# Performance work log

Measured on AMD Instinct MI355X. Metric: run time of the kernel, lower is better.

Reference implementation:

```python
import jax, jax.numpy as jnp
import numpy as np

N, E = 20000, 320000
C, IN_NF, HID_NF, OUT_NF, CH_NF, RAD_NF = 14, 128, 128, 128, 16, 128
CONSTANT = 1.0
LN_EPS = 1e-5
SCALE = 0.02


def _pool_matrix(c, dtype):
    # RollerPooling buffer: pool_matrix[i] averages a sliding window of size c-i
    ones = np.ones((c, c), dtype=np.float32)
    mats = [(np.triu(ones) - np.triu(ones, k=c - i)) / float(c - i) for i in range(c)]
    return jnp.asarray(np.stack(mats), dtype=dtype)


def setup_inputs() -> dict:
    key = jax.random.key(0)
    ks = jax.random.split(key, 32)
    h = jax.random.normal(ks[0], (N, IN_NF), jnp.float32)
    x = jax.random.normal(ks[1], (N, C, 3), jnp.float32)
    row = jax.random.randint(ks[2], (E,), 0, N)
    off = jax.random.randint(ks[3], (E,), 1, N)
    col = (row + off) % N  # guarantees row != col (avoids zero-distance edges)
    channel_attr = jax.random.normal(ks[4], (N, C, CH_NF), jnp.float32)
    w = jax.random.uniform(ks[5], (N, C), jnp.float32, 0.1, 1.0)
    keep = jax.random.uniform(ks[6], (N, C)) > 0.3
    keep = keep.at[:, 0].set(True)  # every node has >=1 active channel
    channel_weights = w * keep.astype(jnp.float32)

    def lin(k, o, i):
        k1, k2 = jax.random.split(k)
        return (jax.random.normal(k1, (o, i), jnp.float32) * SCALE,
                jax.random.normal(k2, (o,), jnp.float32) * SCALE)

    radial_W, radial_b = lin(ks[7], RAD_NF, CH_NF * CH_NF)
    e1_W, e1_b = lin(ks[8], HID_NF, 2 * IN_NF + RAD_NF)
    e2_W, e2_b = lin(ks[9], HID_NF, HID_NF)
    att_W, att_b = lin(ks[10], 1, HID_NF)
    c1_W, c1_b = lin(ks[11], HID_NF, HID_NF)
    c2_W, c2_b = lin(ks[12], C, HID_NF)
    n1_W, n1_b = lin(ks[13], HID_NF, IN_NF + HID_NF)
    n2_W, n2_b = lin(ks[14], OUT_NF, HID_NF)
    ln_g = jnp.ones((OUT_NF,), jnp.float32)
    ln_b = jnp.zeros((OUT_NF,), jnp.float32)
    return dict(h=h, x=x, row=row, col=col, channel_attr=channel_attr,
                channel_weights=channel_weights,
                radial_W=radial_W, radial_b=radial_b,
                e1_W=e1_W, e1_b=e1_b, e2_W=e2_W, e2_b=e2_b,
                att_W=att_W, att_b=att_b,
                c1_W=c1_W, c1_b=c1_b, c2_W=c2_W, c2_b=c2_b,
                n1_W=n1_W, n1_b=n1_b, n2_W=n2_W, n2_b=n2_b,
                ln_g=ln_g, ln_b=ln_b)


def _scatter_mean(v, idx, n):
    s = jnp.zeros((n,) + v.shape[1:], v.dtype).at[idx].add(v)
    cnt = jnp.zeros((n,), v.dtype).at[idx].add(1.0)
    cnt = jnp.maximum(cnt, 1.0)
    return s / cnt.reshape((n,) + (1,) * (v.ndim - 1))


def _forward(h, x, row, col, channel_attr, channel_weights,
             radial_W, radial_b, e1_W, e1_b, e2_W, e2_b, att_W, att_b,
             c1_W, c1_b, c2_W, c2_b, n1_W, n1_b, n2_W, n2_b, ln_g, ln_b):
    n, c, d = x.shape
    silu = jax.nn.silu
    coord_r = x[row]           # [E, C, 3]
    coord_c = x[col]
    # pairwise channel distances [E, C, C]
    dist = jnp.linalg.norm(coord_r[:, :, None, :] - coord_c[:, None, :, :], axis=-1)
    cw_r = channel_weights[row]
    cw_c = channel_weights[col]
    coord_msg = dist * (cw_r[:, :, None] * cw_c[:, None, :])
    # attr_r^T @ coord_msg @ attr_c -> [E, CH_NF, CH_NF]
    radial = jnp.einsum('eca,ecd,edb->eab', channel_attr[row], coord_msg, channel_attr[col])
    radial = radial.reshape(radial.shape[0], -1)
    rnorm = jnp.linalg.norm(radial, axis=-1, keepdims=True) + CONSTANT
    radial = (radial @ radial_W.T + radial_b) / rnorm  # [E, RAD_NF]
    # pooled column coord over active channels
    mask = (channel_weights != 0).astype(x.dtype)      # [N, C]
    csum = mask.sum(-1)                                # [N]
    pooled_col = (coord_c * mask[col][:, :, None]).sum(1) / csum[col][:, None]  # [E, 3]
    coord_diff = coord_r - pooled_col[:, None, :]      # [E, C, 3]
    # edge MLP (dropout = identity in eval)
    ef = jnp.concatenate([h[row], h[col], radial], axis=-1)
    ef = silu(ef @ e1_W.T + e1_b)
    ef = silu(ef @ e2_W.T + e2_b)
    ef = ef * jax.nn.sigmoid(ef @ att_W.T + att_b)     # att_mlp (hidden_nf == input_nf)
    # coord MLP + roller pooling
    ch = silu(ef @ c1_W.T + c1_b) @ c2_W.T + c2_b      # [E, C]
    tsize = csum[row].astype(jnp.int32) - 1            # [E] in [0, C-1]
    pool_mat = _pool_matrix(c, x.dtype)                # [C, C, C]
    pooled = jnp.einsum('eij,ej->ei', pool_mat[tsize], ch)  # [E, C]
    trans = coord_diff * pooled[:, :, None]            # [E, C, 3]
    x_out = x + _scatter_mean(trans, row, n)
    agg = _scatter_mean(ef, col, n)
    nh = jnp.concatenate([h, agg], axis=-1)
    nh = silu(nh @ n1_W.T + n1_b) @ n2_W.T + n2_b
    y = h + nh
    mu = y.mean(-1, keepdims=True)
    var = ((y - mu) ** 2).mean(-1, keepdims=True)
    h_out = (y - mu) / jnp.sqrt(var + LN_EPS) * ln_g + ln_b
    return h_out, x_out


def reference(h, x, row, col, channel_attr, channel_weights,
              radial_W, radial_b, e1_W, e1_b, e2_W, e2_b, att_W, att_b,
              c1_W, c1_b, c2_W, c2_b, n1_W, n1_b, n2_W, n2_b, ln_g, ln_b):
    return _forward(h, x, row, col, channel_attr, channel_weights,
                    radial_W, radial_b, e1_W, e1_b, e2_W, e2_b, att_W, att_b,
                    c1_W, c1_b, c2_W, c2_b, n1_W, n1_b, n2_W, n2_b, ln_g, ln_b)
```

## Files before the change

kernel.cpp:

```cpp
#include <hip/hip_runtime.h>
#include <math.h>

#define NN 20000
#define NE 320000

typedef const float* fp;
typedef short short8 __attribute__((ext_vector_type(8)));
typedef short short4v __attribute__((ext_vector_type(4)));
typedef float f32x4 __attribute__((ext_vector_type(4)));

__device__ __forceinline__ short F2B(float f) {
    unsigned u = __float_as_uint(f);
    return (short)((u + 0x7fffu + ((u >> 16) & 1u)) >> 16);
}
__device__ __forceinline__ short F2Bf(float f) {
    return (short)((__float_as_uint(f) + 0x8000u) >> 16);
}
__device__ __forceinline__ float B2F(short s) {
    return __uint_as_float(((unsigned)(unsigned short)s) << 16);
}
__device__ __forceinline__ float siluf(float v) { return v / (1.f + __expf(-v)); }

#if defined(__has_builtin)
#if __has_builtin(__builtin_amdgcn_mfma_f32_16x16x16bf16_1k)
#define MFMA16_BUILTIN 1
__device__ __forceinline__ f32x4 mfma16(short4v a, short4v b, f32x4 c) {
    return __builtin_amdgcn_mfma_f32_16x16x16bf16_1k(a, b, c, 0, 0, 0);
}
#elif __has_builtin(__builtin_amdgcn_mfma_f32_16x16x16_bf16)
#define MFMA16_BUILTIN 1
__device__ __forceinline__ f32x4 mfma16(short4v a, short4v b, f32x4 c) {
    return __builtin_amdgcn_mfma_f32_16x16x16_bf16(a, b, c, 0, 0, 0);
}
#endif
#endif
#ifndef MFMA16_BUILTIN
__device__ __forceinline__ f32x4 mfma16(short4v a, short4v b, f32x4 c) {
    f32x4 d;
    asm volatile("s_nop 1\n\tv_mfma_f32_16x16x16_bf16 %0, %1, %2, %3\n\ts_nop 7\n\ts_nop 7"
                 : "=v"(d) : "v"(a), "v"(b), "v"(c));
    return d;
}
#endif

__global__ void k_prep_w(fp e1W, fp e2W, fp c1W, fp c2W, fp n1W, fp n2W,
                         short* __restrict__ wb) {
    int i = blockIdx.x * 256 + threadIdx.x;
    if (i >= 149504) return;
    if (i >= 32768 && i < 65536) return;
    float v;
    if (i < 32768)       { int o = i >> 8, k = i & 255; v = e1W[o * 384 + k]; }
    else if (i < 81920)  v = e2W[i - 65536];
    else if (i < 98304)  v = c1W[i - 81920];
    else if (i < 100352) { int q = i - 98304; v = (q < 1792) ? c2W[q] : 0.f; }
    else if (i < 133120) v = n1W[i - 100352];
    else                 v = n2W[i - 133120];
    wb[i] = F2B(v);
}

__global__ void k_fold(fp e1W, fp rW, fp rB, short* __restrict__ wb,
                       float* __restrict__ bc) {
    int o = blockIdx.x, k = threadIdx.x;
    float acc = 0.f;
    for (int m = 0; m < 128; m++) acc += e1W[o * 384 + 256 + m] * rW[m * 256 + k];
    wb[32768 + o * 256 + k] = F2B(acc);
    if (k == 0) {
        float b = 0.f;
        for (int m = 0; m < 128; m++) b += e1W[o * 384 + 256 + m] * rB[m];
        bc[o] = b;
    }
}

__global__ void k_prep_h(fp h, short* __restrict__ hb) {
    int i = blockIdx.x * 256 + threadIdx.x;
    if (i < NN * 128) hb[i] = F2B(h[i]);
}

__global__ void k_prep_attrT(fp attr, fp cw, short* __restrict__ aT) {
    int i = blockIdx.x * 256 + threadIdx.x;
    if (i >= NN * 256) return;
    int n = i >> 8, rem = i & 255, c = rem >> 4, a = rem & 15;
    float v = (c < 14) ? attr[(size_t)n * 224 + c * 16 + a] * cw[n * 14 + c] : 0.f;
    aT[(size_t)n * 256 + a * 16 + c] = F2B(v);
}

__global__ void k_node_pre(fp x, fp cw, float* __restrict__ csum, float* __restrict__ pool) {
    int n = blockIdx.x * blockDim.x + threadIdx.x;
    if (n >= NN) return;
    float cnt = 0.f, px = 0.f, py = 0.f, pz = 0.f;
#pragma unroll
    for (int c = 0; c < 14; c++) {
        float w = cw[n * 14 + c];
        if (w != 0.f) {
            cnt += 1.f;
            px += x[(n * 14 + c) * 3 + 0];
            py += x[(n * 14 + c) * 3 + 1];
            pz += x[(n * 14 + c) * 3 + 2];
        }
    }
    if (cnt < 1.f) cnt = 1.f;
    csum[n] = cnt;
    pool[n * 3 + 0] = px / cnt;
    pool[n * 3 + 1] = py / cnt;
    pool[n * 3 + 2] = pz / cnt;
}

__global__ void k_count(const int* __restrict__ row, const int* __restrict__ col,
                        int* __restrict__ cnt_r, int* __restrict__ cnt_c) {
    int e = blockIdx.x * 256 + threadIdx.x;
    if (e >= NE) return;
    atomicAdd(&cnt_c[col[e]], 1);
    atomicAdd(&cnt_r[row[e]], 1);
}

__global__ void k_scan(int* __restrict__ cnt0, int* __restrict__ cnt1,
                       int* __restrict__ off0, int* __restrict__ off1) {
    __shared__ int part[256];
    const int tid = threadIdx.x;
    for (int a = 0; a < 2; a++) {
        int* cnt = a ? cnt1 : cnt0;
        int* off = a ? off1 : off0;
        int c0 = tid * 79, c1 = c0 + 79;
        if (c1 > 20000) c1 = 20000;
        int s = 0;
        for (int i = c0; i < c1; i++) s += cnt[i];
        part[tid] = s;
        __syncthreads();
        if (tid == 0) {
            int r = 0;
            for (int i = 0; i < 256; i++) { int t = part[i]; part[i] = r; r += t; }
        }
        __syncthreads();
        int run = part[tid];
        for (int i = c0; i < c1; i++) {
            int cv = cnt[i];
            off[i] = run;
            cnt[i] = run;
            run += cv;
        }
        if (tid == 255) off[20000] = run;
        __syncthreads();
    }
}

__global__ void k_fill(const int* __restrict__ row, const int* __restrict__ col,
                       int* __restrict__ head_r, int* __restrict__ head_c,
                       int* __restrict__ eidx_r,
                       int* __restrict__ row_s, int* __restrict__ col_s) {
    int e = blockIdx.x * 256 + threadIdx.x;
    if (e >= NE) return;
    int r = row[e], c = col[e];
    int pc = atomicAdd(&head_c[c], 1);
    row_s[pc] = r;
    col_s[pc] = c;
    int pr = atomicAdd(&head_r[r], 1);
    eidx_r[pr] = pc;
}

__device__ __forceinline__ void gemm_lds(const short* __restrict__ A, int sA,
                                         const short* __restrict__ W, int Ws, int K,
                                         int mt, int nt0, int nts, f32x4* acc) {
    const int lane = threadIdx.x & 63;
    const short* ap = A + (mt * 16 + (lane & 15)) * sA + ((lane >> 4) * 8);
    for (int k0 = 0; k0 < K; k0 += 32) {
        short8 a = *(const short8*)(ap + k0);
#pragma unroll
        for (int t = 0; t < nts; t++) {
            short8 b = *(const short8*)(W + ((nt0 + t) * 16 + (lane & 15)) * Ws + k0 + ((lane >> 4) * 8));
            acc[t] = __builtin_amdgcn_mfma_f32_16x16x32_bf16(a, b, acc[t], 0, 0, 0);
        }
    }
}
__device__ __forceinline__ void gemm_grow(const short* __restrict__ arow,
                                          const short* __restrict__ W, int Ws, int K,
                                          int nt0, int nts, f32x4* acc) {
    const int lane = threadIdx.x & 63;
    for (int k0 = 0; k0 < K; k0 += 32) {
        short8 a = *(const short8*)(arow + k0);
#pragma unroll
        for (int t = 0; t < nts; t++) {
            short8 b = *(const short8*)(W + ((nt0 + t) * 16 + (lane & 15)) * Ws + k0 + ((lane >> 4) * 8));
            acc[t] = __builtin_amdgcn_mfma_f32_16x16x32_bf16(a, b, acc[t], 0, 0, 0);
        }
    }
}

__global__ __launch_bounds__(256, 2) void k_hw(const short* __restrict__ hb,
                                               const short* __restrict__ wb,
                                               short* __restrict__ H12) {
    __shared__ __attribute__((aligned(16))) short A[32 * 136];
    const int tid = threadIdx.x, lane = tid & 63, w = tid >> 6;
    const int bb = lane & 15, quad = lane >> 4;
    const int mt = w & 1, nh = w >> 1, nb0 = blockIdx.x * 32;
    for (int p = tid; p < 512; p += 256) {
        int i = p >> 4, v = p & 15;
        *(short8*)(A + i * 136 + v * 8) = *(const short8*)(hb + (size_t)(nb0 + i) * 128 + v * 8);
    }
    __syncthreads();
    f32x4 acc[4];
#pragma unroll
    for (int t = 0; t < 4; t++) acc[t] = (f32x4){0.f, 0.f, 0.f, 0.f};
    gemm_lds(A, 136, wb, 256, 128, mt, nh * 4, 4, acc);
#pragma unroll
    for (int t = 0; t < 4; t++)
#pragma unroll
        for (int i = 0; i < 4; i++) {
            int m = mt * 16 + quad * 4 + i, n = (nh * 4 + t) * 16 + bb;
            H12[(size_t)(nb0 + m) * 256 + n] = F2Bf(acc[t][i]);
        }
#pragma unroll
    for (int t = 0; t < 4; t++) acc[t] = (f32x4){0.f, 0.f, 0.f, 0.f};
    gemm_lds(A, 136, wb + 128, 256, 128, mt, nh * 4, 4, acc);
#pragma unroll
    for (int t = 0; t < 4; t++)
#pragma unroll
        for (int i = 0; i < 4; i++) {
            int m = mt * 16 + quad * 4 + i, n = (nh * 4 + t) * 16 + bb;
            H12[(size_t)(nb0 + m) * 256 + 128 + n] = F2Bf(acc[t][i]);
        }
}

__global__ __launch_bounds__(256, 7) void k_edge(
    fp x, const int* __restrict__ row_s, const int* __restrict__ col_s,
    const short* __restrict__ attrT, const short* __restrict__ H12,
    const short* __restrict__ wb, const float* __restrict__ bc,
    fp e1B, fp e2B, fp aW, fp aB, fp c1B, fp c2B,
    const float* __restrict__ csum, const float* __restrict__ poolc,
    short* __restrict__ e1p, short* __restrict__ pooledb,
    float* __restrict__ pcrec) {
    __shared__ __attribute__((aligned(16))) short U[8704];
    __shared__ float xc2[4][2][48];
    __shared__ float s_inv[32];
    __shared__ int s_r[32], s_c[32];
    __shared__ float s_ch[32][14];
    __shared__ float s_red8[32][8], s_gate[32];

    const int tid = threadIdx.x, lane = tid & 63, w = tid >> 6;
    const int bb = lane & 15, quad = lane >> 4;
    const int mt = w & 1, nh = w >> 1;
    const int e0 = blockIdx.x * 32;
    const short* Wc = wb + 32768;
    short* Ar = U;
    short* V1 = U;
    short* V2 = U + 4352;

    if (tid < 32) { s_r[tid] = row_s[e0 + tid]; s_c[tid] = col_s[e0 + tid]; }
    __syncthreads();

#pragma unroll 2
    for (int m = 0; m < 8; m++) {
        const int ei = w * 8 + m;
        const int r = s_r[ei], c = s_c[ei];
        const int bufi = m & 1;
        short4v arv = *(const short4v*)(attrT + (size_t)r * 256 + bb * 16 + quad * 4);
        short4v acv = *(const short4v*)(attrT + (size_t)c * 256 + bb * 16 + quad * 4);
        if (lane < 42) xc2[w][bufi][lane] = x[(size_t)c * 42 + lane];
        const int iic = bb < 14 ? bb : 13;
        float xr0 = x[(size_t)r * 42 + iic * 3];
        float xr1 = x[(size_t)r * 42 + iic * 3 + 1];
        float xr2 = x[(size_t)r * 42 + iic * 3 + 2];
        short4v msgv;
#pragma unroll
        for (int t = 0; t < 4; t++) {
            int jj = quad * 4 + t, jc = jj < 14 ? jj : 13;
            float dx = xr0 - xc2[w][bufi][jc * 3];
            float dy = xr1 - xc2[w][bufi][jc * 3 + 1];
            float dz = xr2 - xc2[w][bufi][jc * 3 + 2];
            msgv[t] = F2Bf(sqrtf(dx * dx + dy * dy + dz * dz));
        }
        f32x4 t2 = mfma16(msgv, acv, (f32x4){0.f, 0.f, 0.f, 0.f});
        short4v t2v;
#pragma unroll
        for (int g = 0; g < 4; g++) t2v[g] = F2Bf(t2[g]);
        f32x4 rad = mfma16(arv, t2v, (f32x4){0.f, 0.f, 0.f, 0.f});
        float ss = rad[0] * rad[0] + rad[1] * rad[1] + rad[2] * rad[2] + rad[3] * rad[3];
#pragma unroll
        for (int off = 32; off > 0; off >>= 1) ss += __shfl_xor(ss, off, 64);
        float inv = 1.f / (sqrtf(ss) + 1.f);
        if (lane == 0) s_inv[ei] = inv;
#pragma unroll
        for (int g = 0; g < 4; g++)
            Ar[ei * 264 + (quad * 4 + g) * 16 + bb] = F2Bf(rad[g] * inv);
    }
    __syncthreads();

    f32x4 racc[2][2];
#pragma unroll
    for (int a = 0; a < 2; a++)
#pragma unroll
        for (int b = 0; b < 2; b++) racc[a][b] = (f32x4){0.f, 0.f, 0.f, 0.f};
    for (int k0 = 0; k0 < 256; k0 += 32) {
        short8 a0 = *(const short8*)(Ar + bb * 264 + k0 + quad * 8);
        short8 a1 = *(const short8*)(Ar + (16 + bb) * 264 + k0 + quad * 8);
        short8 b0 = *(const short8*)(Wc + (size_t)(w * 32 + bb) * 256 + k0 + quad * 8);
        short8 b1 = *(const short8*)(Wc + (size_t)(w * 32 + 16 + bb) * 256 + k0 + quad * 8);
        racc[0][0] = __builtin_amdgcn_mfma_f32_16x16x32_bf16(a0, b0, racc[0][0], 0, 0, 0);
        racc[0][1] = __builtin_amdgcn_mfma_f32_16x16x32_bf16(a0, b1, racc[0][1], 0, 0, 0);
        racc[1][0] = __builtin_amdgcn_mfma_f32_16x16x32_bf16(a1, b0, racc[1][0], 0, 0, 0);
        racc[1][1] = __builtin_amdgcn_mfma_f32_16x16x32_bf16(a1, b1, racc[1][1], 0, 0, 0);
    }
    __syncthreads();

#pragma unroll
    for (int a = 0; a < 2; a++)
#pragma unroll
        for (int b = 0; b < 2; b++)
#pragma unroll
            for (int i = 0; i < 4; i++) {
                int m = a * 16 + quad * 4 + i, n = w * 32 + b * 16 + bb;
                V1[m * 136 + n] = F2Bf(racc[a][b][i] + s_inv[m] * bc[n]);
            }
    __syncthreads();

    for (int p = tid; p < 512; p += 256) {
        int e = p >> 4, v = p & 15;
        short8 hr = *(const short8*)(H12 + (size_t)s_r[e] * 256 + v * 8);
        short8 hc = *(const short8*)(H12 + (size_t)s_c[e] * 256 + 128 + v * 8);
        short8 pp = *(const short8*)(V1 + e * 136 + v * 8);
        short8 o;
#pragma unroll
        for (int j = 0; j < 8; j++)
            o[j] = F2Bf(siluf(B2F(hr[j]) + B2F(hc[j]) + B2F(pp[j]) + e1B[v * 8 + j]));
        *(short8*)(V1 + e * 136 + v * 8) = o;
    }
    __syncthreads();

    f32x4 acc[4];
#pragma unroll
    for (int t = 0; t < 4; t++) acc[t] = (f32x4){0.f, 0.f, 0.f, 0.f};
    gemm_lds(V1, 136, wb + 65536, 128, 128, mt, nh * 4, 4, acc);
#pragma unroll
    for (int t = 0; t < 4; t++)
#pragma unroll
        for (int i = 0; i < 4; i++) {
            int m = mt * 16 + quad * 4 + i, n = (nh * 4 + t) * 16 + bb;
            V2[m * 136 + n] = F2Bf(siluf(acc[t][i] + e2B[n]));
        }
    __syncthreads();

    {
        int e = tid >> 3, j = tid & 7;
        float s = 0.f;
        for (int f = j * 16; f < j * 16 + 16; f++) s += B2F(V2[e * 136 + f]) * aW[f];
        s_red8[e][j] = s;
    }
    __syncthreads();
    if (tid < 32) {
        float s = 0.f;
#pragma unroll
        for (int j = 0; j < 8; j++) s += s_red8[tid][j];
        s_gate[tid] = 1.f / (1.f + __expf(-(s + aB[0])));
    }
    __syncthreads();
    for (int p = tid; p < 512; p += 256) {
        int e = p >> 4, v = p & 15;
        short8 a = *(const short8*)(V2 + e * 136 + v * 8);
        short8 o;
#pragma unroll
        for (int j = 0; j < 8; j++) o[j] = F2Bf(B2F(a[j]) * s_gate[e]);
        *(short8*)(V1 + e * 136 + v * 8) = o;
        *(short8*)(e1p + (size_t)(e0 + e) * 128 + v * 8) = o;
    }
    __syncthreads();

#pragma unroll
    for (int t = 0; t < 4; t++) acc[t] = (f32x4){0.f, 0.f, 0.f, 0.f};
    gemm_lds(V1, 136, wb + 81920, 128, 128, mt, nh * 4, 4, acc);
    __syncthreads();
#pragma unroll
    for (int t = 0; t < 4; t++)
#pragma unroll
        for (int i = 0; i < 4; i++) {
            int m = mt * 16 + quad * 4 + i, n = (nh * 4 + t) * 16 + bb;
            V2[m * 136 + n] = F2Bf(siluf(acc[t][i] + c1B[n]));
        }
    __syncthreads();

    if (nh == 0) {
        f32x4 a4 = (f32x4){0.f, 0.f, 0.f, 0.f};
        gemm_lds(V2, 136, wb + 98304, 128, 128, mt, 0, 1, &a4);
#pragma unroll
        for (int i = 0; i < 4; i++) {
            int m = mt * 16 + quad * 4 + i;
            if (bb < 14) s_ch[m][bb] = a4[i] + c2B[bb];
        }
    }
    __syncthreads();

    if (tid < 32) {
        int t = (int)(csum[s_r[tid]] + 0.5f) - 1;
        if (t < 0) t = 0; if (t > 13) t = 13;
        int Wd = 14 - t;
        for (int i = 0; i < 14; i++) {
            int jend = i + Wd - 1; if (jend > 13) jend = 13;
            float a = 0.f;
            for (int j = i; j <= jend; j++) a += s_ch[tid][j];
            pooledb[(size_t)(e0 + tid) * 14 + i] = F2Bf(a / (float)Wd);
        }
        int c = s_c[tid];
        float4 pc = make_float4(poolc[c * 3 + 0], poolc[c * 3 + 1], poolc[c * 3 + 2], 0.f);
        *(float4*)(pcrec + (size_t)(e0 + tid) * 4) = pc;
    }
}

__global__ __launch_bounds__(256, 3) void k_edge_fused(
    fp x, const int* __restrict__ row, const int* __restrict__ col,
    fp attr, fp cw, const short* __restrict__ hb, const short* __restrict__ wb,
    fp e1B, fp e2B, fp aW, fp aB, fp c1B, fp c2B,
    const float* __restrict__ bc, const float* __restrict__ csum,
    const float* __restrict__ poolc,
    float* __restrict__ xacc, float* __restrict__ agg,
    float* __restrict__ cntr, float* __restrict__ cntc) {
    __shared__ __attribute__((aligned(16))) short R1[13056];
    __shared__ float s_xr2[32 * 42];
    __shared__ float T[4][352];
    __shared__ int   s_r[32], s_c[32];
    __shared__ float s_inv[32];
    __shared__ float s_ch[32][14], s_pool[32][14];
    __shared__ float s_red8[32][8];
    __shared__ float s_gate[32];

    const int tid = threadIdx.x, lane = tid & 63, w = tid >> 6;
    const int bb = lane & 15, quad = lane >> 4;

    if (tid < 32) { s_r[tid] = row[blockIdx.x * 32 + tid]; s_c[tid] = col[blockIdx.x * 32 + tid]; }
    __syncthreads();

    float* slot = T[w];
    float* t2w = slot + 72;
    for (int i8 = 0; i8 < 8; i8++) {
        const int e = w * 8 + i8;
        const int r = s_r[e], cl = s_c[e];
        if (lane < 42) {
            s_xr2[e * 42 + lane] = x[(size_t)r * 42 + lane];
            slot[lane] = x[(size_t)cl * 42 + lane];
        }
        if (lane < 14)      slot[42 + lane] = cw[r * 14 + lane];
        else if (lane < 28) slot[56 + (lane - 14)] = cw[cl * 14 + (lane - 14)];
        __builtin_amdgcn_wave_barrier();

        const int iic = bb < 14 ? bb : 13;
        float xr0 = s_xr2[e * 42 + iic * 3], xr1 = s_xr2[e * 42 + iic * 3 + 1],
              xr2v = s_xr2[e * 42 + iic * 3 + 2];
        float cwri = slot[42 + iic];
        short8 msgv, acv;
#pragma unroll
        for (int t = 0; t < 8; t++) {
            int jj = quad * 8 + t, jc = jj < 14 ? jj : 13;
            float dx = xr0 - slot[jc * 3], dy = xr1 - slot[jc * 3 + 1], dz = xr2v - slot[jc * 3 + 2];
            float m = sqrtf(dx * dx + dy * dy + dz * dz) * cwri * slot[56 + jc];
            msgv[t] = (bb < 14 && jj < 14) ? F2B(m) : (short)0;
            acv[t] = F2B(attr[(size_t)cl * 224 + jc * 16 + bb]);
        }
        f32x4 t2 = (f32x4){0.f, 0.f, 0.f, 0.f};
        t2 = __builtin_amdgcn_mfma_f32_16x16x32_bf16(msgv, acv, t2, 0, 0, 0);
#pragma unroll
        for (int g = 0; g < 4; g++) t2w[(quad * 4 + g) * 17 + bb] = t2[g];
        __builtin_amdgcn_wave_barrier();

        short8 arv, t2v;
#pragma unroll
        for (int t = 0; t < 8; t++) {
            int kk = quad * 8 + t, kc = kk < 16 ? kk : 15;
            t2v[t] = F2B(t2w[kc * 17 + bb]);
            arv[t] = (kk < 14) ? F2B(attr[(size_t)r * 224 + kk * 16 + bb]) : (short)0;
        }
        f32x4 rad = (f32x4){0.f, 0.f, 0.f, 0.f};
        rad = __builtin_amdgcn_mfma_f32_16x16x32_bf16(arv, t2v, rad, 0, 0, 0);

        float ss = rad[0] * rad[0] + rad[1] * rad[1] + rad[2] * rad[2] + rad[3] * rad[3];
#pragma unroll
        for (int off = 32; off > 0; off >>= 1) ss += __shfl_xor(ss, off, 64);
        float inv = 1.f / (sqrtf(ss) + 1.f);
        if (lane == 0) s_inv[e] = inv;
#pragma unroll
        for (int g = 0; g < 4; g++)
            R1[e * 264 + (quad * 4 + g) * 16 + bb] = F2B(rad[g] * inv);
        __builtin_amdgcn_wave_barrier();
    }
    __syncthreads();

    const int mt = w & 1, nh = w >> 1;
    const int m_ = mt * 16 + bb;
    f32x4 acc[4];
#pragma unroll
    for (int t = 0; t < 4; t++) acc[t] = (f32x4){0.f, 0.f, 0.f, 0.f};
    {
        const short* ar_ = hb + (size_t)s_r[m_] * 128 + quad * 8;
        const short* ac_ = hb + (size_t)s_c[m_] * 128 + quad * 8;
        gemm_grow(ar_, wb, 256, 128, nh * 4, 4, acc);
        gemm_grow(ac_, wb + 128, 256, 128, nh * 4, 4, acc);
        gemm_lds(R1, 264, wb + 32768, 256, 256, mt, nh * 4, 4, acc);
    }
    __syncthreads();
    short* V1 = R1;
    short* V2 = R1 + 4352;
    short* C1O = R1 + 8704;
#pragma unroll
    for (int t = 0; t < 4; t++)
#pragma unroll
        for (int i = 0; i < 4; i++) {
            int m = mt * 16 + quad * 4 + i, n = (nh * 4 + t) * 16 + bb;
            V1[m * 136 + n] = F2B(siluf(acc[t][i] + e1B[n] + bc[n] * s_inv[m]));
        }
    __syncthreads();

#pragma unroll
    for (int t = 0; t < 4; t++) acc[t] = (f32x4){0.f, 0.f, 0.f, 0.f};
    gemm_lds(V1, 136, wb + 65536, 128, 128, mt, nh * 4, 4, acc);
    __syncthreads();
#pragma unroll
    for (int t = 0; t < 4; t++)
#pragma unroll
        for (int i = 0; i < 4; i++) {
            int m = mt * 16 + quad * 4 + i, n = (nh * 4 + t) * 16 + bb;
            V2[m * 136 + n] = F2B(siluf(acc[t][i] + e2B[n]));
        }
    __syncthreads();

    {
        int e = tid >> 3, j = tid & 7;
        float s = 0.f;
        for (int f = j * 16; f < j * 16 + 16; f++) s += B2F(V2[e * 136 + f]) * aW[f];
        s_red8[e][j] = s;
    }
    __syncthreads();
    if (tid < 32) {
        float s = 0.f;
#pragma unroll
        for (int j = 0; j < 8; j++) s += s_red8[tid][j];
        s_gate[tid] = 1.f / (1.f + __expf(-(s + aB[0])));
    }
    __syncthreads();
    for (int p = tid; p < 32 * 128; p += 256) {
        int e = p >> 7, f = p & 127;
        V1[e * 136 + f] = F2B(B2F(V2[e * 136 + f]) * s_gate[e]);
    }
    __syncthreads();

#pragma unroll
    for (int t = 0; t < 4; t++) acc[t] = (f32x4){0.f, 0.f, 0.f, 0.f};
    gemm_lds(V1, 136, wb + 81920, 128, 128, mt, nh * 4, 4, acc);
    __syncthreads();
#pragma unroll
    for (int t = 0; t < 4; t++)
#pragma unroll
        for (int i = 0; i < 4; i++) {
            int m = mt * 16 + quad * 4 + i, n = (nh * 4 + t) * 16 + bb;
            C1O[m * 136 + n] = F2B(siluf(acc[t][i] + c1B[n]));
        }
    __syncthreads();

    if (nh == 0) {
        f32x4 a4 = (f32x4){0.f, 0.f, 0.f, 0.f};
        gemm_lds(C1O, 136, wb + 98304, 128, 128, mt, 0, 1, &a4);
#pragma unroll
        for (int i = 0; i < 4; i++) {
            int m = mt * 16 + quad * 4 + i;
            if (bb < 14) s_ch[m][bb] = a4[i] + c2B[bb];
        }
    }
    __syncthreads();

    if (tid < 32) {
        int t = (int)(csum[s_r[tid]] + 0.5f) - 1;
        if (t < 0) t = 0; if (t > 13) t = 13;
        int Wd = 14 - t;
        for (int i = 0; i < 14; i++) {
            int jend = i + Wd - 1; if (jend > 13) jend = 13;
            float a = 0.f;
            for (int j = i; j <= jend; j++) a += s_ch[tid][j];
            s_pool[tid][i] = a / (float)Wd;
        }
    }
    __syncthreads();

    for (int p = tid; p < 32 * 42; p += 256) {
        int e = p / 42, q = p - e * 42, i = q / 3, d = q - i * 3;
        float diff = s_xr2[e * 42 + q] - poolc[s_c[e] * 3 + d];
        atomicAdd(&xacc[(size_t)s_r[e] * 42 + q], diff * s_pool[e][i]);
    }
    for (int p = tid; p < 32 * 128; p += 256) {
        int e = p >> 7, f = p & 127;
        atomicAdd(&agg[(size_t)s_c[e] * 128 + f], B2F(V1[e * 136 + f]));
    }
    if (tid < 32) {
        atomicAdd(&cntr[s_r[tid]], 1.f);
        atomicAdd(&cntc[s_c[tid]], 1.f);
    }
}

__global__ __launch_bounds__(256, 4) void k_node_post_csr(
    fp h, fp x, const short* __restrict__ wb,
    fp n1B, fp n2B, fp lng, fp lnb,
    const short* __restrict__ efb, const short* __restrict__ pooledb,
    const int* __restrict__ off_c, const int* __restrict__ off_r,
    const int* __restrict__ eidx_r, const float* __restrict__ pcrec,
    float* __restrict__ outh, float* __restrict__ outx) {
    __shared__ __attribute__((aligned(16))) short nA[32 * 264];
    __shared__ __attribute__((aligned(16))) short nMid[32 * 136];
    __shared__ float nred8[32][8];
    __shared__ float nmu[32], nrs[32];
    float* nY = (float*)nA;

    const int tid = threadIdx.x;
    const int wave = tid >> 6, mt = wave & 1, nh = wave >> 1;
    const int lane = tid & 63, bb = lane & 15, quad = lane >> 4;
    const int nb0 = blockIdx.x * 32;
    const short* n1Wb = wb + 100352;
    const short* n2Wb = wb + 133120;

    for (int p = tid; p < 32 * 128; p += 256) {
        int i = p >> 7, f = p & 127;
        nA[i * 264 + f] = F2Bf(h[(size_t)(nb0 + i) * 128 + f]);
    }
    {
        const int ni = tid >> 3, seg = tid & 7;
        const int n = nb0 + ni;
        const int beg = off_c[n], end = off_c[n + 1];
        float av[16];
#pragma unroll
        for (int j = 0; j < 16; j++) av[j] = 0.f;
        for (int k = beg; k < end; k++) {
            short8 u0 = *(const short8*)(efb + (size_t)k * 128 + seg * 16);
            short8 u1 = *(const short8*)(efb + (size_t)k * 128 + seg * 16 + 8);
#pragma unroll
            for (int j = 0; j < 8; j++) { av[j] += B2F(u0[j]); av[8 + j] += B2F(u1[j]); }
        }
        float inv = 1.f / fmaxf((float)(end - beg), 1.f);
#pragma unroll
        for (int j = 0; j < 16; j++)
            nA[ni * 264 + 128 + seg * 16 + j] = F2Bf(av[j] * inv);
    }
    __syncthreads();

    f32x4 acc[4];
#pragma unroll
    for (int t = 0; t < 4; t++) acc[t] = (f32x4){0.f, 0.f, 0.f, 0.f};
    gemm_lds(nA, 264, n1Wb, 256, 256, mt, nh * 4, 4, acc);
#pragma unroll
    for (int t = 0; t < 4; t++)
#pragma unroll
        for (int i = 0; i < 4; i++) {
            int m = mt * 16 + quad * 4 + i, n = (nh * 4 + t) * 16 + bb;
            nMid[m * 136 + n] = F2Bf(siluf(acc[t][i] + n1B[n]));
        }
    __syncthreads();

#pragma unroll
    for (int t = 0; t < 4; t++) acc[t] = (f32x4){0.f, 0.f, 0.f, 0.f};
    gemm_lds(nMid, 136, n2Wb, 128, 128, mt, nh * 4, 4, acc);
#pragma unroll
    for (int t = 0; t < 4; t++)
#pragma unroll
        for (int i = 0; i < 4; i++) {
            int m = mt * 16 + quad * 4 + i, n = (nh * 4 + t) * 16 + bb;
            nY[m * 128 + n] = acc[t][i] + n2B[n] + h[(size_t)(nb0 + m) * 128 + n];
        }
    __syncthreads();

    {
        int i = tid >> 3, j = tid & 7;
        float s = 0.f;
        for (int f = j * 16; f < j * 16 + 16; f++) s += nY[i * 128 + f];
        nred8[i][j] = s;
    }
    __syncthreads();
    if (tid < 32) {
        float s = 0.f;
#pragma unroll
        for (int j = 0; j < 8; j++) s += nred8[tid][j];
        nmu[tid] = s * (1.f / 128.f);
    }
    __syncthreads();
    {
        int i = tid >> 3, j = tid & 7;
        float mu = nmu[i], s = 0.f;
        for (int f = j * 16; f < j * 16 + 16; f++) { float d = nY[i * 128 + f] - mu; s += d * d; }
        nred8[i][j] = s;
    }
    __syncthreads();
    if (tid < 32) {
        float s = 0.f;
#pragma unroll
        for (int j = 0; j < 8; j++) s += nred8[tid][j];
        nrs[tid] = rsqrtf(s * (1.f / 128.f) + 1e-5f);
    }
    __syncthreads();
    for (int p = tid; p < 32 * 128; p += 256) {
        int i = p >> 7, f = p & 127;
        outh[(size_t)(nb0 + i) * 128 + f] = (nY[i * 128 + f] - nmu[i]) * nrs[i] * lng[f] + lnb[f];
    }
    for (int p = tid; p < 32 * 3; p += 256) {
        int i = p / 3, d = p - i * 3;
        int n = nb0 + i;
        int beg = off_r[n], end = off_r[n + 1];
        float Q[14], P[14];
#pragma unroll
        for (int ic = 0; ic < 14; ic++) { Q[ic] = 0.f; P[ic] = 0.f; }
        for (int k = beg; k < end; k++) {
            int sp = eidx_r[k];
            const int* pp = (const int*)(pooledb + (size_t)sp * 14);
            float4 pc = *(const float4*)(pcrec + (size_t)sp * 4);
            float pcd = (d == 0) ? pc.x : ((d == 1) ? pc.y : pc.z);
#pragma unroll
            for (int u2 = 0; u2 < 7; u2++) {
                int u = pp[u2];
                float pw0 = B2F((short)(u & 0xffff));
                float pw1 = B2F((short)(((unsigned)u) >> 16));
                P[2 * u2] += pw0;     Q[2 * u2] += pw0 * pcd;
                P[2 * u2 + 1] += pw1; Q[2 * u2 + 1] += pw1 * pcd;
            }
        }
        float invd = 1.f / fmaxf((float)(end - beg), 1.f);
#pragma unroll
        for (int ic = 0; ic < 14; ic++) {
            float x0 = x[(size_t)n * 42 + ic * 3 + d];
            outx[(size_t)n * 42 + ic * 3 + d] = x0 + (x0 * P[ic] - Q[ic]) * invd;
        }
    }
}

__global__ __launch_bounds__(256, 2) void k_node_post(
    fp h, fp x, const short* __restrict__ wb,
    fp n1B, fp n2B, fp lng, fp lnb,
    const float* __restrict__ agg, const float* __restrict__ cntc,
    const float* __restrict__ xacc, const float* __restrict__ cntr,
    float* __restrict__ outh, float* __restrict__ outx) {
    __shared__ __attribute__((aligned(16))) short nA[32 * 264];
    __shared__ __attribute__((aligned(16))) short nMid[32 * 136];
    __shared__ float nY[32][128];
    __shared__ float nred8[32][8];
    __shared__ float nmu[32], nrs[32];

    const int tid = threadIdx.x;
    const int wave = tid >> 6, mt = wave & 1, nh = wave >> 1;
    const int lane = tid & 63, bb = lane & 15, quad = lane >> 4;
    const int nb0 = blockIdx.x * 32;
    const short* n1Wb = wb + 100352;
    const short* n2Wb = wb + 133120;

    for (int p = tid; p < 32 * 128; p += 256) {
        int i = p >> 7, f = p & 127;
        int n = nb0 + i;
        nA[i * 264 + f] = F2Bf(h[(size_t)n * 128 + f]);
        float cc = cntc[n]; if (cc < 1.f) cc = 1.f;
        nA[i * 264 + 128 + f] = F2Bf(agg[(size_t)n * 128 + f] / cc);
    }
    __syncthreads();

    f32x4 acc[4];
#pragma unroll
    for (int t = 0; t < 4; t++) acc[t] = (f32x4){0.f, 0.f, 0.f, 0.f};
    gemm_lds(nA, 264, n1Wb, 256, 256, mt, nh * 4, 4, acc);
#pragma unroll
    for (int t = 0; t < 4; t++)
#pragma unroll
        for (int i = 0; i < 4; i++) {
            int m = mt * 16 + quad * 4 + i, n = (nh * 4 + t) * 16 + bb;
            nMid[m * 136 + n] = F2Bf(siluf(acc[t][i] + n1B[n]));
        }
    __syncthreads();

#pragma unroll
    for (int t = 0; t < 4; t++) acc[t] = (f32x4){0.f, 0.f, 0.f, 0.f};
    gemm_lds(nMid, 136, n2Wb, 128, 128, mt, nh * 4, 4, acc);
#pragma unroll
    for (int t = 0; t < 4; t++)
#pragma unroll
        for (int i = 0; i < 4; i++) {
            int m = mt * 16 + quad * 4 + i, n = (nh * 4 + t) * 16 + bb;
            nY[m][n] = acc[t][i] + n2B[n] + h[(size_t)(nb0 + m) * 128 + n];
        }
    __syncthreads();

    {
        int i = tid >> 3, j = tid & 7;
        float s = 0.f;
        for (int f = j * 16; f < j * 16 + 16; f++) s += nY[i][f];
        nred8[i][j] = s;
    }
    __syncthreads();
    if (tid < 32) {
        float s = 0.f;
#pragma unroll
        for (int j = 0; j < 8; j++) s += nred8[tid][j];
        nmu[tid] = s * (1.f / 128.f);
    }
    __syncthreads();
    {
        int i = tid >> 3, j = tid & 7;
        float mu = nmu[i], s = 0.f;
        for (int f = j * 16; f < j * 16 + 16; f++) { float d = nY[i][f] - mu; s += d * d; }
        nred8[i][j] = s;
    }
    __syncthreads();
    if (tid < 32) {
        float s = 0.f;
#pragma unroll
        for (int j = 0; j < 8; j++) s += nred8[tid][j];
        nrs[tid] = rsqrtf(s * (1.f / 128.f) + 1e-5f);
    }
    __syncthreads();
    for (int p = tid; p < 32 * 128; p += 256) {
        int i = p >> 7, f = p & 127;
        outh[(size_t)(nb0 + i) * 128 + f] = (nY[i][f] - nmu[i]) * nrs[i] * lng[f] + lnb[f];
    }
    for (int p = tid; p < 32 * 42; p += 256) {
        int i = p / 42, q = p - i * 42;
        int n = nb0 + i;
        float cr = cntr[n]; if (cr < 1.f) cr = 1.f;
        outx[(size_t)n * 42 + q] = x[(size_t)n * 42 + q] + xacc[(size_t)n * 42 + q] / cr;
    }
}

extern "C" void kernel_launch(void* const* d_in, const int* in_sizes, int n_in,
                              void* d_out, int out_size, void* d_ws, size_t ws_size,
                              hipStream_t stream) {
    fp h   = (fp)d_in[0];
    fp x   = (fp)d_in[1];
    const int* row = (const int*)d_in[2];
    const int* col = (const int*)d_in[3];
    fp attr= (fp)d_in[4];
    fp cw  = (fp)d_in[5];
    fp rW  = (fp)d_in[6];  fp rB  = (fp)d_in[7];
    fp e1W = (fp)d_in[8];  fp e1B = (fp)d_in[9];
    fp e2W = (fp)d_in[10]; fp e2B = (fp)d_in[11];
    fp aW  = (fp)d_in[12]; fp aB  = (fp)d_in[13];
    fp c1W = (fp)d_in[14]; fp c1B = (fp)d_in[15];
    fp c2W = (fp)d_in[16]; fp c2B = (fp)d_in[17];
    fp n1W = (fp)d_in[18]; fp n1B = (fp)d_in[19];
    fp n2W = (fp)d_in[20]; fp n2B = (fp)d_in[21];
    fp lng = (fp)d_in[22]; fp lnb = (fp)d_in[23];

    float* ws    = (float*)d_ws;
    int*   wsi   = (int*)d_ws;
    float* xacc  = ws;
    float* agg   = ws + 840000;
    float* cntr  = ws + 3400000;
    float* cntc  = ws + 3420000;
    float* csum  = ws + 3440000;
    float* pool  = ws + 3460000;
    float* bc    = ws + 3520000;
    short* hb    = (short*)(ws + 3520128);
    short* wb    = (short*)(ws + 4800128);
    short* H12   = (short*)(ws + 4874880);
    short* e1p   = (short*)(ws + 7434880);
    short* attrT = (short*)(ws + 27914880);
    short* pooledb = (short*)(ws + 1040004);
    float* pcrec   = ws + 3520128;

    int* off_c  = wsi + 0;
    int* off_r  = wsi + 20002;
    int* head_c = wsi + 40004;
    int* head_r = wsi + 60004;
    int* eidx_r = wsi + 80004;
    int* row_s  = wsi + 400004;
    int* col_s  = wsi + 720004;

    const size_t need = 30474880ull * 4ull;

    if (ws_size >= need) {
        hipMemsetAsync(head_c, 0, 40000 * sizeof(int), stream);
        k_count<<<(NE + 255) / 256, 256, 0, stream>>>(row, col, head_r, head_c);
        k_scan<<<1, 256, 0, stream>>>(head_c, head_r, off_c, off_r);
        k_fill<<<(NE + 255) / 256, 256, 0, stream>>>(row, col, head_r, head_c,
                                                     eidx_r, row_s, col_s);

        k_prep_w<<<(149504 + 255) / 256, 256, 0, stream>>>(e1W, e2W, c1W, c2W, n1W, n2W, wb);
        k_fold<<<128, 256, 0, stream>>>(e1W, rW, rB, wb, bc);
        k_prep_h<<<(NN * 128 + 255) / 256, 256, 0, stream>>>(h, hb);
        k_node_pre<<<(NN + 255) / 256, 256, 0, stream>>>(x, cw, csum, pool);
        k_prep_attrT<<<(NN * 256 + 255) / 256, 256, 0, stream>>>(attr, cw, attrT);
        k_hw<<<NN / 32, 256, 0, stream>>>(hb, wb, H12);
        k_edge<<<NE / 32, 256, 0, stream>>>(x, row_s, col_s, attrT, H12, wb, bc,
                                            e1B, e2B, aW, aB, c1B, c2B,
                                            csum, pool, e1p, pooledb, pcrec);
        float* outh = (float*)d_out;
        float* outx = outh + NN * 128;
        k_node_post_csr<<<NN / 32, 256, 0, stream>>>(h, x, wb, n1B, n2B, lng, lnb,
                                                     e1p, pooledb,
                                                     off_c, off_r, eidx_r,
                                                     pcrec, outh, outx);
    } else {
        hipMemsetAsync(d_ws, 0, 3440000 * sizeof(float), stream);
        k_prep_w<<<(149504 + 255) / 256, 256, 0, stream>>>(e1W, e2W, c1W, c2W, n1W, n2W, wb);
        k_fold<<<128, 256, 0, stream>>>(e1W, rW, rB, wb, bc);
        k_prep_h<<<(NN * 128 + 255) / 256, 256, 0, stream>>>(h, hb);
        k_node_pre<<<(NN + 255) / 256, 256, 0, stream>>>(x, cw, csum, pool);
        k_edge_fused<<<NE / 32, 256, 0, stream>>>(x, row, col, attr, cw, hb, wb,
                                                  e1B, e2B, aW, aB, c1B, c2B,
                                                  bc, csum, pool, xacc, agg, cntr, cntc);
        float* outh = (float*)d_out;
        float* outx = outh + NN * 128;
        k_node_post<<<NN / 32, 256, 0, stream>>>(h, x, wb, n1B, n2B, lng, lnb,
                                                 agg, cntc, xacc, cntr, outh, outx);
    }
}
```

Baseline: 704.1 us.

## Merge prep kernels into one launch, fold gate into c1 epilogue, vectorize x loads

Six small preprocessing kernels (count, weight prep, fold, h cast, node pre, attr transpose) are merged into a single launch that dispatches on block index, cutting launch overhead and serialization gaps. In the edge kernel, the attention gate is applied after the c1 GEMM as a per-row scale (algebraically equivalent), so the GEMM can start without waiting for the gated copy, which removes a barrier and one LDS round-trip. Column-node coordinates are now read with vector loads straight into registers instead of being staged through shared memory. The gate scaling now happens in fp32 on the accumulator instead of on bf16-rounded inputs, which slightly changes rounding.

```diff
diff --git a/kernel.cpp b/kernel.cpp
--- a/kernel.cpp
+++ b/kernel.cpp
@@ -20,6 +20,11 @@
     return __uint_as_float(((unsigned)(unsigned short)s) << 16);
 }
 __device__ __forceinline__ float siluf(float v) { return v / (1.f + __expf(-v)); }
+__device__ __forceinline__ f32x4 ld4(const float* p) {
+    f32x4 v;
+    __builtin_memcpy(&v, p, 16);
+    return v;
+}
 
 #if defined(__has_builtin)
 #if __has_builtin(__builtin_amdgcn_mfma_f32_16x16x16bf16_1k)
@@ -105,12 +110,87 @@
     pool[n * 3 + 2] = pz / cnt;
 }
 
-__global__ void k_count(const int* __restrict__ row, const int* __restrict__ col,
-                        int* __restrict__ cnt_r, int* __restrict__ cnt_c) {
-    int e = blockIdx.x * 256 + threadIdx.x;
-    if (e >= NE) return;
-    atomicAdd(&cnt_c[col[e]], 1);
-    atomicAdd(&cnt_r[row[e]], 1);
+__global__ void k_prep_all(fp e1W, fp e2W, fp c1W, fp c2W, fp n1W, fp n2W,
+                           fp rW, fp rB, fp h, fp x, fp attr, fp cw,
+                           const int* __restrict__ row, const int* __restrict__ col,
+                           short* __restrict__ wb, float* __restrict__ bc,
+                           short* __restrict__ hb,
+                           float* __restrict__ csum, float* __restrict__ pool,
+                           short* __restrict__ aT,
+                           int* __restrict__ cnt_r, int* __restrict__ cnt_c) {
+    int b = blockIdx.x;
+    const int tid = threadIdx.x;
+    if (b < 1250) {
+        int e = b * 256 + tid;
+        if (e < NE) {
+            atomicAdd(&cnt_c[col[e]], 1);
+            atomicAdd(&cnt_r[row[e]], 1);
+        }
+        return;
+    }
+    b -= 1250;
+    if (b < 584) {
+        int i = b * 256 + tid;
+        if (i >= 149504) return;
+        if (i >= 32768 && i < 65536) return;
+        float v;
+        if (i < 32768)       { int o = i >> 8, k = i & 255; v = e1W[o * 384 + k]; }
+        else if (i < 81920)  v = e2W[i - 65536];
+        else if (i < 98304)  v = c1W[i - 81920];
+        else if (i < 100352) { int q = i - 98304; v = (q < 1792) ? c2W[q] : 0.f; }
+        else if (i < 133120) v = n1W[i - 100352];
+        else                 v = n2W[i - 133120];
+        wb[i] = F2B(v);
+        return;
+    }
+    b -= 584;
+    if (b < 128) {
+        int o = b, k = tid;
+        float acc = 0.f;
+        for (int m = 0; m < 128; m++) acc += e1W[o * 384 + 256 + m] * rW[m * 256 + k];
+        wb[32768 + o * 256 + k] = F2B(acc);
+        if (k == 0) {
+            float bsum = 0.f;
+            for (int m = 0; m < 128; m++) bsum += e1W[o * 384 + 256 + m] * rB[m];
+            bc[o] = bsum;
+        }
+        return;
+    }
+    b -= 128;
+    if (b < 10000) {
+        int i = b * 256 + tid;
+        hb[i] = F2B(h[i]);
+        return;
+    }
+    b -= 10000;
+    if (b < 79) {
+        int n = b * 256 + tid;
+        if (n >= NN) return;
+        float cnt = 0.f, px = 0.f, py = 0.f, pz = 0.f;
+#pragma unroll
+        for (int c = 0; c < 14; c++) {
+            float w = cw[n * 14 + c];
+            if (w != 0.f) {
+                cnt += 1.f;
+                px += x[(n * 14 + c) * 3 + 0];
+                py += x[(n * 14 + c) * 3 + 1];
+                pz += x[(n * 14 + c) * 3 + 2];
+            }
+        }
+        if (cnt < 1.f) cnt = 1.f;
+        csum[n] = cnt;
+        pool[n * 3 + 0] = px / cnt;
+        pool[n * 3 + 1] = py / cnt;
+        pool[n * 3 + 2] = pz / cnt;
+        return;
+    }
+    b -= 79;
+    {
+        int i = b * 256 + tid;
+        int n = i >> 8, rem = i & 255, c = rem >> 4, a = rem & 15;
+        float v = (c < 14) ? attr[(size_t)n * 224 + c * 16 + a] * cw[n * 14 + c] : 0.f;
+        aT[(size_t)n * 256 + a * 16 + c] = F2B(v);
+    }
 }
 
 __global__ void k_scan(int* __restrict__ cnt0, int* __restrict__ cnt1,
@@ -229,7 +309,6 @@
     short* __restrict__ e1p, short* __restrict__ pooledb,
     float* __restrict__ pcrec) {
     __shared__ __attribute__((aligned(16))) short U[8704];
-    __shared__ float xc2[4][2][48];
     __shared__ float s_inv[32];
     __shared__ int s_r[32], s_c[32];
     __shared__ float s_ch[32][14];
@@ -247,25 +326,28 @@
     if (tid < 32) { s_r[tid] = row_s[e0 + tid]; s_c[tid] = col_s[e0 + tid]; }
     __syncthreads();
 
+    const int iic = bb < 14 ? bb : 13;
+    const bool q3 = (quad == 3);
+    const int cb = q3 ? 30 : quad * 12;
 #pragma unroll 2
     for (int m = 0; m < 8; m++) {
         const int ei = w * 8 + m;
         const int r = s_r[ei], c = s_c[ei];
-        const int bufi = m & 1;
         short4v arv = *(const short4v*)(attrT + (size_t)r * 256 + bb * 16 + quad * 4);
         short4v acv = *(const short4v*)(attrT + (size_t)c * 256 + bb * 16 + quad * 4);
-        if (lane < 42) xc2[w][bufi][lane] = x[(size_t)c * 42 + lane];
-        const int iic = bb < 14 ? bb : 13;
-        float xr0 = x[(size_t)r * 42 + iic * 3];
-        float xr1 = x[(size_t)r * 42 + iic * 3 + 1];
-        float xr2 = x[(size_t)r * 42 + iic * 3 + 2];
+        const float* xrp = x + (size_t)r * 42 + iic * 3;
+        float xr0 = xrp[0], xr1 = xrp[1], xr2 = xrp[2];
+        const float* xcp = x + (size_t)c * 42 + cb;
+        f32x4 L0 = ld4(xcp), L1 = ld4(xcp + 4), L2 = ld4(xcp + 8);
+        float cxv[4], cyv[4], czv[4];
+        cxv[0] = q3 ? L1[2] : L0[0]; cyv[0] = q3 ? L1[3] : L0[1]; czv[0] = q3 ? L2[0] : L0[2];
+        cxv[1] = q3 ? L2[1] : L0[3]; cyv[1] = q3 ? L2[2] : L1[0]; czv[1] = q3 ? L2[3] : L1[1];
+        cxv[2] = q3 ? L2[1] : L1[2]; cyv[2] = q3 ? L2[2] : L1[3]; czv[2] = q3 ? L2[3] : L2[0];
+        cxv[3] = L2[1];              cyv[3] = L2[2];              czv[3] = L2[3];
         short4v msgv;
 #pragma unroll
         for (int t = 0; t < 4; t++) {
-            int jj = quad * 4 + t, jc = jj < 14 ? jj : 13;
-            float dx = xr0 - xc2[w][bufi][jc * 3];
-            float dy = xr1 - xc2[w][bufi][jc * 3 + 1];
-            float dz = xr2 - xc2[w][bufi][jc * 3 + 2];
+            float dx = xr0 - cxv[t], dy = xr1 - cyv[t], dz = xr2 - czv[t];
             msgv[t] = F2Bf(sqrtf(dx * dx + dy * dy + dz * dz));
         }
         f32x4 t2 = mfma16(msgv, acv, (f32x4){0.f, 0.f, 0.f, 0.f});
@@ -351,34 +433,31 @@
         for (int j = 0; j < 8; j++) s += s_red8[tid][j];
         s_gate[tid] = 1.f / (1.f + __expf(-(s + aB[0])));
     }
-    __syncthreads();
+#pragma unroll
+    for (int t = 0; t < 4; t++) acc[t] = (f32x4){0.f, 0.f, 0.f, 0.f};
+    gemm_lds(V2, 136, wb + 81920, 128, 128, mt, nh * 4, 4, acc);
+    __syncthreads();
+
+#pragma unroll
+    for (int t = 0; t < 4; t++)
+#pragma unroll
+        for (int i = 0; i < 4; i++) {
+            int m = mt * 16 + quad * 4 + i, n = (nh * 4 + t) * 16 + bb;
+            V1[m * 136 + n] = F2Bf(siluf(s_gate[m] * acc[t][i] + c1B[n]));
+        }
     for (int p = tid; p < 512; p += 256) {
         int e = p >> 4, v = p & 15;
         short8 a = *(const short8*)(V2 + e * 136 + v * 8);
         short8 o;
 #pragma unroll
         for (int j = 0; j < 8; j++) o[j] = F2Bf(B2F(a[j]) * s_gate[e]);
-        *(short8*)(V1 + e * 136 + v * 8) = o;
         *(short8*)(e1p + (size_t)(e0 + e) * 128 + v * 8) = o;
     }
-    __syncthreads();
-
-#pragma unroll
-    for (int t = 0; t < 4; t++) acc[t] = (f32x4){0.f, 0.f, 0.f, 0.f};
-    gemm_lds(V1, 136, wb + 81920, 128, 128, mt, nh * 4, 4, acc);
-    __syncthreads();
-#pragma unroll
-    for (int t = 0; t < 4; t++)
-#pragma unroll
-        for (int i = 0; i < 4; i++) {
-            int m = mt * 16 + quad * 4 + i, n = (nh * 4 + t) * 16 + bb;
-            V2[m * 136 + n] = F2Bf(siluf(acc[t][i] + c1B[n]));
-        }
     __syncthreads();
 
     if (nh == 0) {
         f32x4 a4 = (f32x4){0.f, 0.f, 0.f, 0.f};
-        gemm_lds(V2, 136, wb + 98304, 128, 128, mt, 0, 1, &a4);
+        gemm_lds(V1, 136, wb + 98304, 128, 128, mt, 0, 1, &a4);
 #pragma unroll
         for (int i = 0; i < 4; i++) {
             int m = mt * 16 + quad * 4 + i;
@@ -862,16 +941,13 @@
 
     if (ws_size >= need) {
         hipMemsetAsync(head_c, 0, 40000 * sizeof(int), stream);
-        k_count<<<(NE + 255) / 256, 256, 0, stream>>>(row, col, head_r, head_c);
+        k_prep_all<<<32041, 256, 0, stream>>>(e1W, e2W, c1W, c2W, n1W, n2W,
+                                              rW, rB, h, x, attr, cw, row, col,
+                                              wb, bc, hb, csum, pool, attrT,
+                                              head_r, head_c);
         k_scan<<<1, 256, 0, stream>>>(head_c, head_r, off_c, off_r);
         k_fill<<<(NE + 255) / 256, 256, 0, stream>>>(row, col, head_r, head_c,
                                                      eidx_r, row_s, col_s);
-
-        k_prep_w<<<(149504 + 255) / 256, 256, 0, stream>>>(e1W, e2W, c1W, c2W, n1W, n2W, wb);
-        k_fold<<<128, 256, 0, stream>>>(e1W, rW, rB, wb, bc);
-        k_prep_h<<<(NN * 128 + 255) / 256, 256, 0, stream>>>(h, hb);
-        k_node_pre<<<(NN + 255) / 256, 256, 0, stream>>>(x, cw, csum, pool);
-        k_prep_attrT<<<(NN * 256 + 255) / 256, 256, 0, stream>>>(attr, cw, attrT);
         k_hw<<<NN / 32, 256, 0, stream>>>(hb, wb, H12);
         k_edge<<<NE / 32, 256, 0, stream>>>(x, row_s, col_s, attrT, H12, wb, bc,
                                             e1B, e2B, aW, aB, c1B, c2B,
```

Result: faster. 686.6 us (-2.5%).
